# Optimization experiments

Measured on AMD Instinct MI355X. Metric: run time of the kernel, lower is better.

The kernel has to match this reference:

```python
import jax, jax.numpy as jnp
import numpy as np

B, DZ, DS, DH = 8192, 1024, 64, 4096

def setup_inputs() -> dict:
    key = jax.random.key(0)
    ks = jax.random.split(key, 8)
    r1 = 1.0 / np.sqrt(DZ)   # W1 init range (last dim dz)
    r2 = 1.0 / np.sqrt(DH)   # W2 init range (last dim dim_hidden)
    rc = 1.0 / np.sqrt(DS)   # C init range
    return {
        "z": jax.random.normal(ks[0], (B, DZ), jnp.float32),
        "s": jax.random.normal(ks[1], (B, DS), jnp.float32),
        "A": jnp.full((DZ,), 0.95, jnp.float32),
        "W1": jax.random.uniform(ks[2], (DH, DZ), jnp.float32, -r1, r1),
        "W2": jax.random.uniform(ks[3], (DZ, DH), jnp.float32, -r2, r2),
        "h1": jax.random.normal(ks[4], (DH,), jnp.float32),
        "h2": jax.random.normal(ks[5], (DZ,), jnp.float32),
        "C": jax.random.uniform(ks[6], (DZ, DS), jnp.float32, -rc, rc),
    }

def reference(z, s, A, W1, W2, h1, h2, C):
    # PLRNN step, W_trial=False, mean_center=False, noise=0:
    # z' = A*z + relu(z @ W1.T + h1) @ W2.T + h2 + s @ C.T
    z_activated = jax.nn.relu(z @ W1.T + h1)          # [B, DH]
    return A * z + z_activated @ W2.T + h2 + s @ C.T  # [B, DZ]
```

## Files before the change

### kernel.cpp

```cpp
#include <hip/hip_runtime.h>

#define BB 8192
#define DZ 1024
#define DS 64
#define DH 4096
#define KEXT (DH + DS)

typedef float floatx4 __attribute__((ext_vector_type(4)));
typedef __bf16 bf16x8 __attribute__((ext_vector_type(8)));
typedef __attribute__((address_space(1))) void* as1_void_ptr;
typedef __attribute__((address_space(3))) void* as3_void_ptr;

__device__ __forceinline__ void async_copy16(const void* g, void* l) {
    __builtin_amdgcn_global_load_lds((as1_void_ptr)g, (as3_void_ptr)l, 16, 0, 0);
}

__global__ void prep_all(const float* __restrict__ z, const float* __restrict__ W1,
                         const float* __restrict__ W2, const float* __restrict__ C,
                         const float* __restrict__ s,
                         __bf16* __restrict__ zb, __bf16* __restrict__ W1b,
                         __bf16* __restrict__ B2b, __bf16* __restrict__ Hb) {
    const int b = blockIdx.x, t = threadIdx.x;
    if (b < 8192) {
        int i = b * 256 + t;
        float4 v = ((const float4*)z)[i];
        __bf16* o = zb + (size_t)i * 4;
        o[0] = (__bf16)v.x; o[1] = (__bf16)v.y; o[2] = (__bf16)v.z; o[3] = (__bf16)v.w;
    } else if (b < 12288) {
        int i = (b - 8192) * 256 + t;
        float4 v = ((const float4*)W1)[i];
        __bf16* o = W1b + (size_t)i * 4;
        o[0] = (__bf16)v.x; o[1] = (__bf16)v.y; o[2] = (__bf16)v.z; o[3] = (__bf16)v.w;
    } else if (b < 13312) {
        int j = b - 12288;
        for (int h = t; h < KEXT; h += 256) {
            float v = (h < DH) ? W2[(size_t)j * DH + h] : C[(size_t)j * DS + (h - DH)];
            B2b[(size_t)j * KEXT + h] = (__bf16)v;
        }
    } else {
        int i = (b - 13312) * 256 + t;
        int r = i >> 6, k = i & 63;
        Hb[(size_t)r * KEXT + DH + k] = (__bf16)s[i];
    }
}


__global__ __launch_bounds__(256) void gemm1_relu(
    const __bf16* __restrict__ Ag, const __bf16* __restrict__ Bg,
    const float* __restrict__ h1, __bf16* __restrict__ Hb)
{
    constexpr int ldA = DZ, ldB = DZ, KITER = DZ / 64;
    __shared__ __align__(16) __bf16 As[2 * 128 * 32];
    __shared__ __align__(16) __bf16 Bs[2 * 128 * 32];

    const int tid = threadIdx.x;
    const int wave = tid >> 6, lane = tid & 63;
    const int wm = wave >> 1, wn = wave & 1;
    const int row0 = blockIdx.x * 128;
    const int col0 = blockIdx.y * 128;

    const __bf16* pA = Ag + (size_t)(row0 + (tid >> 2)) * ldA + (tid & 3) * 8;
    const __bf16* pB = Bg + (size_t)(col0 + (tid >> 2)) * ldB + (tid & 3) * 8;
    __bf16* dA0 = As + wave * 16 * 32;
    __bf16* dB0 = Bs + wave * 16 * 32;

    const __bf16* Afrag = As + (wm * 64 + (lane & 15)) * 32 + (lane >> 4) * 8;
    const __bf16* Bfrag = Bs + (wn * 64 + (lane & 15)) * 32 + (lane >> 4) * 8;

    floatx4 acc[4][4];
#pragma unroll
    for (int i = 0; i < 4; ++i)
#pragma unroll
        for (int j = 0; j < 4; ++j) acc[i][j] = (floatx4)0.0f;

    for (int kt = 0; kt < KITER; ++kt) {
        const __bf16* ak = pA + kt * 64;
        const __bf16* bk = pB + kt * 64;
        async_copy16(ak,                         dA0);
        async_copy16(ak + (size_t)64 * ldA,      dA0 + 64 * 32);
        async_copy16(ak + 32,                    dA0 + 128 * 32);
        async_copy16(ak + (size_t)64 * ldA + 32, dA0 + 128 * 32 + 64 * 32);
        async_copy16(bk,                         dB0);
        async_copy16(bk + (size_t)64 * ldB,      dB0 + 64 * 32);
        async_copy16(bk + 32,                    dB0 + 128 * 32);
        async_copy16(bk + (size_t)64 * ldB + 32, dB0 + 128 * 32 + 64 * 32);
        __builtin_amdgcn_s_waitcnt(0);
        __syncthreads();

#pragma unroll
        for (int ks = 0; ks < 2; ++ks) {
            bf16x8 af[4], bfr[4];
#pragma unroll
            for (int i = 0; i < 4; ++i) af[i] = *(const bf16x8*)(Afrag + ks * 4096 + i * 16 * 32);
#pragma unroll
            for (int j = 0; j < 4; ++j) bfr[j] = *(const bf16x8*)(Bfrag + ks * 4096 + j * 16 * 32);
#pragma unroll
            for (int i = 0; i < 4; ++i)
#pragma unroll
                for (int j = 0; j < 4; ++j)
                    acc[i][j] = __builtin_amdgcn_mfma_f32_16x16x32_bf16(af[i], bfr[j], acc[i][j], 0, 0, 0);
        }
        __syncthreads();
    }

    const int r0 = row0 + wm * 64 + (lane >> 4) * 4;
    const int c0 = col0 + wn * 64 + (lane & 15);
#pragma unroll
    for (int i = 0; i < 4; ++i) {
#pragma unroll
        for (int j = 0; j < 4; ++j) {
            int c = c0 + j * 16;
            float bias = h1[c];
#pragma unroll
            for (int rg = 0; rg < 4; ++rg) {
                int r = r0 + i * 16 + rg;
                float v = acc[i][j][rg] + bias;
                v = v > 0.0f ? v : 0.0f;
                Hb[(size_t)r * KEXT + c] = (__bf16)v;
            }
        }
    }
}

__global__ __launch_bounds__(256) void gemm2_out(
    const __bf16* __restrict__ Ag, const __bf16* __restrict__ Bg,
    const float* __restrict__ Adiag, const float* __restrict__ h2,
    const __bf16* __restrict__ zb, float* __restrict__ out)
{
    constexpr int ldA = KEXT, ldB = KEXT, KITER = KEXT / 64;
    __shared__ __align__(16) __bf16 As[2 * 128 * 32];
    __shared__ __align__(16) __bf16 Bs[2 * 128 * 32];

    const int tid = threadIdx.x;
    const int wave = tid >> 6, lane = tid & 63;
    const int wm = wave >> 1, wn = wave & 1;
    const int row0 = blockIdx.x * 128;
    const int col0 = blockIdx.y * 128;

    const __bf16* pA = Ag + (size_t)(row0 + (tid >> 2)) * ldA + (tid & 3) * 8;
    const __bf16* pB = Bg + (size_t)(col0 + (tid >> 2)) * ldB + (tid & 3) * 8;
    __bf16* dA0 = As + wave * 16 * 32;
    __bf16* dB0 = Bs + wave * 16 * 32;

    const __bf16* Afrag = As + (wm * 64 + (lane & 15)) * 32 + (lane >> 4) * 8;
    const __bf16* Bfrag = Bs + (wn * 64 + (lane & 15)) * 32 + (lane >> 4) * 8;

    floatx4 acc[4][4];
#pragma unroll
    for (int i = 0; i < 4; ++i)
#pragma unroll
        for (int j = 0; j < 4; ++j) acc[i][j] = (floatx4)0.0f;

    for (int kt = 0; kt < KITER; ++kt) {
        const __bf16* ak = pA + kt * 64;
        const __bf16* bk = pB + kt * 64;
        async_copy16(ak,                         dA0);
        async_copy16(ak + (size_t)64 * ldA,      dA0 + 64 * 32);
        async_copy16(ak + 32,                    dA0 + 128 * 32);
        async_copy16(ak + (size_t)64 * ldA + 32, dA0 + 128 * 32 + 64 * 32);
        async_copy16(bk,                         dB0);
        async_copy16(bk + (size_t)64 * ldB,      dB0 + 64 * 32);
        async_copy16(bk + 32,                    dB0 + 128 * 32);
        async_copy16(bk + (size_t)64 * ldB + 32, dB0 + 128 * 32 + 64 * 32);
        __builtin_amdgcn_s_waitcnt(0);
        __syncthreads();

#pragma unroll
        for (int ks = 0; ks < 2; ++ks) {
            bf16x8 af[4], bfr[4];
#pragma unroll
            for (int i = 0; i < 4; ++i) af[i] = *(const bf16x8*)(Afrag + ks * 4096 + i * 16 * 32);
#pragma unroll
            for (int j = 0; j < 4; ++j) bfr[j] = *(const bf16x8*)(Bfrag + ks * 4096 + j * 16 * 32);
#pragma unroll
            for (int i = 0; i < 4; ++i)
#pragma unroll
                for (int j = 0; j < 4; ++j)
                    acc[i][j] = __builtin_amdgcn_mfma_f32_16x16x32_bf16(af[i], bfr[j], acc[i][j], 0, 0, 0);
        }
        __syncthreads();
    }

    const int r0 = row0 + wm * 64 + (lane >> 4) * 4;
    const int c0 = col0 + wn * 64 + (lane & 15);
#pragma unroll
    for (int i = 0; i < 4; ++i) {
#pragma unroll
        for (int j = 0; j < 4; ++j) {
            const int c = c0 + j * 16;
            const float aj = Adiag[c];
            const float hj = h2[c];
#pragma unroll
            for (int rg = 0; rg < 4; ++rg) {
                const int r = r0 + i * 16 + rg;
                out[(size_t)r * DZ + c] =
                    acc[i][j][rg] + aj * (float)zb[(size_t)r * DZ + c] + hj;
            }
        }
    }
}


extern "C" void kernel_launch(void* const* d_in, const int* in_sizes, int n_in,
                              void* d_out, int out_size, void* d_ws, size_t ws_size,
                              hipStream_t stream) {
    const float* z  = (const float*)d_in[0];
    const float* s  = (const float*)d_in[1];
    const float* A  = (const float*)d_in[2];
    const float* W1 = (const float*)d_in[3];
    const float* W2 = (const float*)d_in[4];
    const float* h1 = (const float*)d_in[5];
    const float* h2 = (const float*)d_in[6];
    const float* C  = (const float*)d_in[7];
    float* out = (float*)d_out;

    char* ws = (char*)d_ws;
    size_t offHb  = 0;
    size_t offZb  = offHb  + (size_t)BB * KEXT * 2;
    size_t offW1b = offZb  + (size_t)BB * DZ * 2;
    size_t offB2b = offW1b + (size_t)DH * DZ * 2;
    __bf16* Hb  = (__bf16*)(ws + offHb);
    __bf16* zb  = (__bf16*)(ws + offZb);
    __bf16* W1b = (__bf16*)(ws + offW1b);
    __bf16* B2b = (__bf16*)(ws + offB2b);

    prep_all<<<15360, 256, 0, stream>>>(z, W1, W2, C, s, zb, W1b, B2b, Hb);
    gemm1_relu<<<dim3(BB / 128, DH / 128), 256, 0, stream>>>(zb, W1b, h1, Hb);
    gemm2_out<<<dim3(BB / 128, DZ / 128), 256, 0, stream>>>(Hb, B2b, A, h2, zb, out);
}
```

Baseline: 282.2 us.

## Double-buffer GEMM K-loop with swizzled LDS and 32x32 MFMA tiles

Both GEMM kernels now share a pipelined mainloop that prefetches the next 32-wide K slice into an alternate LDS buffer while computing on the current one, waiting on a partial vmcnt instead of draining all loads. The LDS layout uses an XOR chunk swizzle to reduce bank conflicts on fragment reads, and the MFMA switches from 16x16x32 to 32x32x16 with a 2x2 accumulator grid per wave. The epilogues are remapped to the 32x32 output layout. The goal is to hide global-load latency and cut LDS traffic per MFMA, at the cost of halving K per iteration (more barriers) and relying on hand-encoded waitcnt constants.

```diff
diff --git a/kernel.cpp b/kernel.cpp
--- a/kernel.cpp
+++ b/kernel.cpp
@@ -6,10 +6,14 @@
 #define DH 4096
 #define KEXT (DH + DS)
 
-typedef float floatx4 __attribute__((ext_vector_type(4)));
+typedef float floatx16 __attribute__((ext_vector_type(16)));
 typedef __bf16 bf16x8 __attribute__((ext_vector_type(8)));
 typedef __attribute__((address_space(1))) void* as1_void_ptr;
 typedef __attribute__((address_space(3))) void* as3_void_ptr;
+
+#define WAIT_VM4   3956
+#define WAIT_VM0   3952
+#define WAIT_LGKM0 49279
 
 __device__ __forceinline__ void async_copy16(const void* g, void* l) {
     __builtin_amdgcn_global_load_lds((as1_void_ptr)g, (as3_void_ptr)l, 16, 0, 0);
@@ -45,78 +49,94 @@
 }
 
 
+
+#define GEMM_PIPELINE_BODY(KITER_, ldA_, ldB_)                                          \
+    const int tid = threadIdx.x;                                                        \
+    const int wave = tid >> 6, lane = tid & 63;                                         \
+    const int wm = wave >> 1, wn = wave & 1;                                            \
+    const int row0 = blockIdx.x * 128;                                                  \
+    const int col0 = blockIdx.y * 128;                                                  \
+    const int srow = tid >> 2;                                   \
+    const int schk = (tid & 3) ^ (srow & 3);                 \
+    const __bf16* pA = Ag + (size_t)(row0 + srow) * ldA_ + schk * 8;                    \
+    const __bf16* pB = Bg + (size_t)(col0 + srow) * ldB_ + schk * 8;                    \
+    const int mA = lane & 31, hA = lane >> 5;                                           \
+    floatx16 acc[2][2];                                                                 \
+    acc[0][0] = (floatx16)0.0f; acc[0][1] = (floatx16)0.0f;                             \
+    acc[1][0] = (floatx16)0.0f; acc[1][1] = (floatx16)0.0f;                             \
+    {                                         \
+        __bf16* lA = As + wave * 512;                                                   \
+        __bf16* lB = Bs + wave * 512;                                                   \
+        async_copy16(pA,                    lA);                                        \
+        async_copy16(pA + (size_t)64*ldA_,  lA + 2048);                                 \
+        async_copy16(pB,                    lB);                                        \
+        async_copy16(pB + (size_t)64*ldB_,  lB + 2048);                                 \
+    }                                                                                   \
+    for (int kt = 0; kt < KITER_; ++kt) {                                               \
+        const int p = kt & 1;                                                           \
+        if (kt + 1 < KITER_) {                                                          \
+            const __bf16* ak = pA + (kt + 1) * 32;                                      \
+            const __bf16* bk = pB + (kt + 1) * 32;                                      \
+            __bf16* lA = As + (p ^ 1) * 4096 + wave * 512;                              \
+            __bf16* lB = Bs + (p ^ 1) * 4096 + wave * 512;                              \
+            async_copy16(ak,                    lA);                                    \
+            async_copy16(ak + (size_t)64*ldA_,  lA + 2048);                             \
+            async_copy16(bk,                    lB);                                    \
+            async_copy16(bk + (size_t)64*ldB_,  lB + 2048);                             \
+            __builtin_amdgcn_s_waitcnt(WAIT_VM4);                                       \
+        } else {                                                                        \
+            __builtin_amdgcn_s_waitcnt(WAIT_VM0);                                       \
+        }                                                                               \
+        __builtin_amdgcn_s_barrier();                                                   \
+        const __bf16* Ab = As + p * 4096;                                               \
+        const __bf16* Bb = Bs + p * 4096;                                               \
+        _Pragma("unroll")                                                               \
+        for (int ks = 0; ks < 2; ++ks) {                                                \
+            bf16x8 af[2], bf[2];                                                        \
+            _Pragma("unroll")                                                           \
+            for (int i = 0; i < 2; ++i) {                                               \
+                int r = wm * 64 + i * 32 + mA;                                          \
+                int chunk = (ks * 2 + hA) ^ (mA & 3);                                   \
+                af[i] = *(const bf16x8*)(Ab + r * 32 + chunk * 8);                      \
+            }                                                                           \
+            _Pragma("unroll")                                                           \
+            for (int j = 0; j < 2; ++j) {                                               \
+                int r = wn * 64 + j * 32 + mA;                                          \
+                int chunk = (ks * 2 + hA) ^ (mA & 3);                                   \
+                bf[j] = *(const bf16x8*)(Bb + r * 32 + chunk * 8);                      \
+            }                                                                           \
+            _Pragma("unroll")                                                           \
+            for (int i = 0; i < 2; ++i)                                                 \
+                _Pragma("unroll")                                                       \
+                for (int j = 0; j < 2; ++j)                                             \
+                    acc[i][j] = __builtin_amdgcn_mfma_f32_32x32x16_bf16(                \
+                        af[i], bf[j], acc[i][j], 0, 0, 0);                              \
+        }                                                                               \
+        __builtin_amdgcn_s_waitcnt(WAIT_LGKM0);                                         \
+        __builtin_amdgcn_s_barrier();                                                   \
+    }
+
 __global__ __launch_bounds__(256) void gemm1_relu(
     const __bf16* __restrict__ Ag, const __bf16* __restrict__ Bg,
     const float* __restrict__ h1, __bf16* __restrict__ Hb)
 {
-    constexpr int ldA = DZ, ldB = DZ, KITER = DZ / 64;
     __shared__ __align__(16) __bf16 As[2 * 128 * 32];
     __shared__ __align__(16) __bf16 Bs[2 * 128 * 32];
 
-    const int tid = threadIdx.x;
-    const int wave = tid >> 6, lane = tid & 63;
-    const int wm = wave >> 1, wn = wave & 1;
-    const int row0 = blockIdx.x * 128;
-    const int col0 = blockIdx.y * 128;
-
-    const __bf16* pA = Ag + (size_t)(row0 + (tid >> 2)) * ldA + (tid & 3) * 8;
-    const __bf16* pB = Bg + (size_t)(col0 + (tid >> 2)) * ldB + (tid & 3) * 8;
-    __bf16* dA0 = As + wave * 16 * 32;
-    __bf16* dB0 = Bs + wave * 16 * 32;
-
-    const __bf16* Afrag = As + (wm * 64 + (lane & 15)) * 32 + (lane >> 4) * 8;
-    const __bf16* Bfrag = Bs + (wn * 64 + (lane & 15)) * 32 + (lane >> 4) * 8;
-
-    floatx4 acc[4][4];
-#pragma unroll
-    for (int i = 0; i < 4; ++i)
-#pragma unroll
-        for (int j = 0; j < 4; ++j) acc[i][j] = (floatx4)0.0f;
-
-    for (int kt = 0; kt < KITER; ++kt) {
-        const __bf16* ak = pA + kt * 64;
-        const __bf16* bk = pB + kt * 64;
-        async_copy16(ak,                         dA0);
-        async_copy16(ak + (size_t)64 * ldA,      dA0 + 64 * 32);
-        async_copy16(ak + 32,                    dA0 + 128 * 32);
-        async_copy16(ak + (size_t)64 * ldA + 32, dA0 + 128 * 32 + 64 * 32);
-        async_copy16(bk,                         dB0);
-        async_copy16(bk + (size_t)64 * ldB,      dB0 + 64 * 32);
-        async_copy16(bk + 32,                    dB0 + 128 * 32);
-        async_copy16(bk + (size_t)64 * ldB + 32, dB0 + 128 * 32 + 64 * 32);
-        __builtin_amdgcn_s_waitcnt(0);
-        __syncthreads();
+    GEMM_PIPELINE_BODY(32, DZ, DZ)
 
 #pragma unroll
-        for (int ks = 0; ks < 2; ++ks) {
-            bf16x8 af[4], bfr[4];
+    for (int i = 0; i < 2; ++i) {
 #pragma unroll
-            for (int i = 0; i < 4; ++i) af[i] = *(const bf16x8*)(Afrag + ks * 4096 + i * 16 * 32);
+        for (int j = 0; j < 2; ++j) {
+            const int cbase = col0 + wn * 64 + j * 32 + mA;
+            const float bias = h1[cbase];
 #pragma unroll
-            for (int j = 0; j < 4; ++j) bfr[j] = *(const bf16x8*)(Bfrag + ks * 4096 + j * 16 * 32);
-#pragma unroll
-            for (int i = 0; i < 4; ++i)
-#pragma unroll
-                for (int j = 0; j < 4; ++j)
-                    acc[i][j] = __builtin_amdgcn_mfma_f32_16x16x32_bf16(af[i], bfr[j], acc[i][j], 0, 0, 0);
-        }
-        __syncthreads();
-    }
-
-    const int r0 = row0 + wm * 64 + (lane >> 4) * 4;
-    const int c0 = col0 + wn * 64 + (lane & 15);
-#pragma unroll
-    for (int i = 0; i < 4; ++i) {
-#pragma unroll
-        for (int j = 0; j < 4; ++j) {
-            int c = c0 + j * 16;
-            float bias = h1[c];
-#pragma unroll
-            for (int rg = 0; rg < 4; ++rg) {
-                int r = r0 + i * 16 + rg;
+            for (int rg = 0; rg < 16; ++rg) {
+                const int r = row0 + wm * 64 + i * 32 + (rg & 3) + 8 * (rg >> 2) + 4 * hA;
                 float v = acc[i][j][rg] + bias;
                 v = v > 0.0f ? v : 0.0f;
-                Hb[(size_t)r * KEXT + c] = (__bf16)v;
+                Hb[(size_t)r * KEXT + cbase] = (__bf16)v;
             }
         }
     }
@@ -127,72 +147,21 @@
     const float* __restrict__ Adiag, const float* __restrict__ h2,
     const __bf16* __restrict__ zb, float* __restrict__ out)
 {
-    constexpr int ldA = KEXT, ldB = KEXT, KITER = KEXT / 64;
     __shared__ __align__(16) __bf16 As[2 * 128 * 32];
     __shared__ __align__(16) __bf16 Bs[2 * 128 * 32];
 
-    const int tid = threadIdx.x;
-    const int wave = tid >> 6, lane = tid & 63;
-    const int wm = wave >> 1, wn = wave & 1;
-    const int row0 = blockIdx.x * 128;
-    const int col0 = blockIdx.y * 128;
-
-    const __bf16* pA = Ag + (size_t)(row0 + (tid >> 2)) * ldA + (tid & 3) * 8;
-    const __bf16* pB = Bg + (size_t)(col0 + (tid >> 2)) * ldB + (tid & 3) * 8;
-    __bf16* dA0 = As + wave * 16 * 32;
-    __bf16* dB0 = Bs + wave * 16 * 32;
-
-    const __bf16* Afrag = As + (wm * 64 + (lane & 15)) * 32 + (lane >> 4) * 8;
-    const __bf16* Bfrag = Bs + (wn * 64 + (lane & 15)) * 32 + (lane >> 4) * 8;
-
-    floatx4 acc[4][4];
-#pragma unroll
-    for (int i = 0; i < 4; ++i)
-#pragma unroll
-        for (int j = 0; j < 4; ++j) acc[i][j] = (floatx4)0.0f;
-
-    for (int kt = 0; kt < KITER; ++kt) {
-        const __bf16* ak = pA + kt * 64;
-        const __bf16* bk = pB + kt * 64;
-        async_copy16(ak,                         dA0);
-        async_copy16(ak + (size_t)64 * ldA,      dA0 + 64 * 32);
-        async_copy16(ak + 32,                    dA0 + 128 * 32);
-        async_copy16(ak + (size_t)64 * ldA + 32, dA0 + 128 * 32 + 64 * 32);
-        async_copy16(bk,                         dB0);
-        async_copy16(bk + (size_t)64 * ldB,      dB0 + 64 * 32);
-        async_copy16(bk + 32,                    dB0 + 128 * 32);
-        async_copy16(bk + (size_t)64 * ldB + 32, dB0 + 128 * 32 + 64 * 32);
-        __builtin_amdgcn_s_waitcnt(0);
-        __syncthreads();
+    GEMM_PIPELINE_BODY(130, KEXT, KEXT)
 
 #pragma unroll
-        for (int ks = 0; ks < 2; ++ks) {
-            bf16x8 af[4], bfr[4];
+    for (int i = 0; i < 2; ++i) {
 #pragma unroll
-            for (int i = 0; i < 4; ++i) af[i] = *(const bf16x8*)(Afrag + ks * 4096 + i * 16 * 32);
-#pragma unroll
-            for (int j = 0; j < 4; ++j) bfr[j] = *(const bf16x8*)(Bfrag + ks * 4096 + j * 16 * 32);
-#pragma unroll
-            for (int i = 0; i < 4; ++i)
-#pragma unroll
-                for (int j = 0; j < 4; ++j)
-                    acc[i][j] = __builtin_amdgcn_mfma_f32_16x16x32_bf16(af[i], bfr[j], acc[i][j], 0, 0, 0);
-        }
-        __syncthreads();
-    }
-
-    const int r0 = row0 + wm * 64 + (lane >> 4) * 4;
-    const int c0 = col0 + wn * 64 + (lane & 15);
-#pragma unroll
-    for (int i = 0; i < 4; ++i) {
-#pragma unroll
-        for (int j = 0; j < 4; ++j) {
-            const int c = c0 + j * 16;
+        for (int j = 0; j < 2; ++j) {
+            const int c = col0 + wn * 64 + j * 32 + mA;
             const float aj = Adiag[c];
             const float hj = h2[c];
 #pragma unroll
-            for (int rg = 0; rg < 4; ++rg) {
-                const int r = r0 + i * 16 + rg;
+            for (int rg = 0; rg < 16; ++rg) {
+                const int r = row0 + wm * 64 + i * 32 + (rg & 3) + 8 * (rg >> 2) + 4 * hA;
                 out[(size_t)r * DZ + c] =
                     acc[i][j][rg] + aj * (float)zb[(size_t)r * DZ + c] + hj;
             }
```

Result: slower. 304.7 us (+8.0%).

## Double-buffer LDS tiles with async prefetch in both GEMM kernels

Applied to the files above, without the earlier changes.

Both GEMM main loops now prefetch the next K-tile into a second LDS buffer with global_load_lds, then wait only on older vmem loads via partial vmcnt waits before a raw barrier. gemm1 switches to 32-wide K steps so its double-buffered tile fits the existing LDS allocation, while gemm2 doubles its LDS to hold two 64-wide K-tiles. The aim is to overlap global-to-LDS copies with MFMA work instead of fully draining memory every iteration. The risks are fragile hand-encoded waitcnt constants, more barriers per K in gemm1, and higher LDS use in gemm2 that may reduce occupancy.

```diff
diff --git a/kernel.cpp b/kernel.cpp
--- a/kernel.cpp
+++ b/kernel.cpp
@@ -10,6 +10,11 @@
 typedef __bf16 bf16x8 __attribute__((ext_vector_type(8)));
 typedef __attribute__((address_space(1))) void* as1_void_ptr;
 typedef __attribute__((address_space(3))) void* as3_void_ptr;
+
+#define WAIT_VM0   3952
+#define WAIT_VM4   3956
+#define WAIT_VM8   3960
+#define WAIT_LGKM0 49279
 
 __device__ __forceinline__ void async_copy16(const void* g, void* l) {
     __builtin_amdgcn_global_load_lds((as1_void_ptr)g, (as3_void_ptr)l, 16, 0, 0);
@@ -49,7 +54,7 @@
     const __bf16* __restrict__ Ag, const __bf16* __restrict__ Bg,
     const float* __restrict__ h1, __bf16* __restrict__ Hb)
 {
-    constexpr int ldA = DZ, ldB = DZ, KITER = DZ / 64;
+    constexpr int ldA = DZ, ldB = DZ, KITER = DZ / 32;
     __shared__ __align__(16) __bf16 As[2 * 128 * 32];
     __shared__ __align__(16) __bf16 Bs[2 * 128 * 32];
 
@@ -61,8 +66,6 @@
 
     const __bf16* pA = Ag + (size_t)(row0 + (tid >> 2)) * ldA + (tid & 3) * 8;
     const __bf16* pB = Bg + (size_t)(col0 + (tid >> 2)) * ldB + (tid & 3) * 8;
-    __bf16* dA0 = As + wave * 16 * 32;
-    __bf16* dB0 = Bs + wave * 16 * 32;
 
     const __bf16* Afrag = As + (wm * 64 + (lane & 15)) * 32 + (lane >> 4) * 8;
     const __bf16* Bfrag = Bs + (wn * 64 + (lane & 15)) * 32 + (lane >> 4) * 8;
@@ -73,34 +76,47 @@
 #pragma unroll
         for (int j = 0; j < 4; ++j) acc[i][j] = (floatx4)0.0f;
 
+    {
+        __bf16* lA = As + wave * 512;
+        __bf16* lB = Bs + wave * 512;
+        async_copy16(pA,                        lA);
+        async_copy16(pA + (size_t)64 * ldA,     lA + 2048);
+        async_copy16(pB,                        lB);
+        async_copy16(pB + (size_t)64 * ldB,     lB + 2048);
+    }
+
     for (int kt = 0; kt < KITER; ++kt) {
-        const __bf16* ak = pA + kt * 64;
-        const __bf16* bk = pB + kt * 64;
-        async_copy16(ak,                         dA0);
-        async_copy16(ak + (size_t)64 * ldA,      dA0 + 64 * 32);
-        async_copy16(ak + 32,                    dA0 + 128 * 32);
-        async_copy16(ak + (size_t)64 * ldA + 32, dA0 + 128 * 32 + 64 * 32);
-        async_copy16(bk,                         dB0);
-        async_copy16(bk + (size_t)64 * ldB,      dB0 + 64 * 32);
-        async_copy16(bk + 32,                    dB0 + 128 * 32);
-        async_copy16(bk + (size_t)64 * ldB + 32, dB0 + 128 * 32 + 64 * 32);
-        __builtin_amdgcn_s_waitcnt(0);
-        __syncthreads();
-
-#pragma unroll
-        for (int ks = 0; ks < 2; ++ks) {
-            bf16x8 af[4], bfr[4];
-#pragma unroll
-            for (int i = 0; i < 4; ++i) af[i] = *(const bf16x8*)(Afrag + ks * 4096 + i * 16 * 32);
-#pragma unroll
-            for (int j = 0; j < 4; ++j) bfr[j] = *(const bf16x8*)(Bfrag + ks * 4096 + j * 16 * 32);
-#pragma unroll
-            for (int i = 0; i < 4; ++i)
-#pragma unroll
-                for (int j = 0; j < 4; ++j)
-                    acc[i][j] = __builtin_amdgcn_mfma_f32_16x16x32_bf16(af[i], bfr[j], acc[i][j], 0, 0, 0);
-        }
-        __syncthreads();
+        const int p = kt & 1;
+        if (kt + 1 < KITER) {
+            const __bf16* ak = pA + (kt + 1) * 32;
+            const __bf16* bk = pB + (kt + 1) * 32;
+            __bf16* lA = As + (p ^ 1) * 4096 + wave * 512;
+            __bf16* lB = Bs + (p ^ 1) * 4096 + wave * 512;
+            async_copy16(ak,                    lA);
+            async_copy16(ak + (size_t)64 * ldA, lA + 2048);
+            async_copy16(bk,                    lB);
+            async_copy16(bk + (size_t)64 * ldB, lB + 2048);
+            __builtin_amdgcn_s_waitcnt(WAIT_VM4);
+        } else {
+            __builtin_amdgcn_s_waitcnt(WAIT_VM0);
+        }
+        __builtin_amdgcn_s_barrier();
+
+        const __bf16* Ab = Afrag + p * 4096;
+        const __bf16* Bb = Bfrag + p * 4096;
+        bf16x8 af[4], bfr[4];
+#pragma unroll
+        for (int i = 0; i < 4; ++i) af[i] = *(const bf16x8*)(Ab + i * 16 * 32);
+#pragma unroll
+        for (int j = 0; j < 4; ++j) bfr[j] = *(const bf16x8*)(Bb + j * 16 * 32);
+#pragma unroll
+        for (int i = 0; i < 4; ++i)
+#pragma unroll
+            for (int j = 0; j < 4; ++j)
+                acc[i][j] = __builtin_amdgcn_mfma_f32_16x16x32_bf16(af[i], bfr[j], acc[i][j], 0, 0, 0);
+
+        __builtin_amdgcn_s_waitcnt(WAIT_LGKM0);
+        __builtin_amdgcn_s_barrier();
     }
 
     const int r0 = row0 + wm * 64 + (lane >> 4) * 4;
@@ -128,8 +144,8 @@
     const __bf16* __restrict__ zb, float* __restrict__ out)
 {
     constexpr int ldA = KEXT, ldB = KEXT, KITER = KEXT / 64;
-    __shared__ __align__(16) __bf16 As[2 * 128 * 32];
-    __shared__ __align__(16) __bf16 Bs[2 * 128 * 32];
+    __shared__ __align__(16) __bf16 As[2 * 2 * 128 * 32];
+    __shared__ __align__(16) __bf16 Bs[2 * 2 * 128 * 32];
 
     const int tid = threadIdx.x;
     const int wave = tid >> 6, lane = tid & 63;
@@ -139,8 +155,6 @@
 
     const __bf16* pA = Ag + (size_t)(row0 + (tid >> 2)) * ldA + (tid & 3) * 8;
     const __bf16* pB = Bg + (size_t)(col0 + (tid >> 2)) * ldB + (tid & 3) * 8;
-    __bf16* dA0 = As + wave * 16 * 32;
-    __bf16* dB0 = Bs + wave * 16 * 32;
 
     const __bf16* Afrag = As + (wm * 64 + (lane & 15)) * 32 + (lane >> 4) * 8;
     const __bf16* Bfrag = Bs + (wn * 64 + (lane & 15)) * 32 + (lane >> 4) * 8;
@@ -151,34 +165,58 @@
 #pragma unroll
         for (int j = 0; j < 4; ++j) acc[i][j] = (floatx4)0.0f;
 
+    {
+        __bf16* lA = As + wave * 512;
+        __bf16* lB = Bs + wave * 512;
+        async_copy16(pA,                             lA);
+        async_copy16(pA + (size_t)64 * ldA,          lA + 2048);
+        async_copy16(pA + 32,                        lA + 4096);
+        async_copy16(pA + (size_t)64 * ldA + 32,     lA + 4096 + 2048);
+        async_copy16(pB,                             lB);
+        async_copy16(pB + (size_t)64 * ldB,          lB + 2048);
+        async_copy16(pB + 32,                        lB + 4096);
+        async_copy16(pB + (size_t)64 * ldB + 32,     lB + 4096 + 2048);
+    }
+
     for (int kt = 0; kt < KITER; ++kt) {
-        const __bf16* ak = pA + kt * 64;
-        const __bf16* bk = pB + kt * 64;
-        async_copy16(ak,                         dA0);
-        async_copy16(ak + (size_t)64 * ldA,      dA0 + 64 * 32);
-        async_copy16(ak + 32,                    dA0 + 128 * 32);
-        async_copy16(ak + (size_t)64 * ldA + 32, dA0 + 128 * 32 + 64 * 32);
-        async_copy16(bk,                         dB0);
-        async_copy16(bk + (size_t)64 * ldB,      dB0 + 64 * 32);
-        async_copy16(bk + 32,                    dB0 + 128 * 32);
-        async_copy16(bk + (size_t)64 * ldB + 32, dB0 + 128 * 32 + 64 * 32);
-        __builtin_amdgcn_s_waitcnt(0);
-        __syncthreads();
+        const int p = kt & 1;
+        if (kt + 1 < KITER) {
+            const __bf16* ak = pA + (kt + 1) * 64;
+            const __bf16* bk = pB + (kt + 1) * 64;
+            __bf16* lA = As + (p ^ 1) * 8192 + wave * 512;
+            __bf16* lB = Bs + (p ^ 1) * 8192 + wave * 512;
+            async_copy16(ak,                         lA);
+            async_copy16(ak + (size_t)64 * ldA,      lA + 2048);
+            async_copy16(ak + 32,                    lA + 4096);
+            async_copy16(ak + (size_t)64 * ldA + 32, lA + 4096 + 2048);
+            async_copy16(bk,                         lB);
+            async_copy16(bk + (size_t)64 * ldB,      lB + 2048);
+            async_copy16(bk + 32,                    lB + 4096);
+            async_copy16(bk + (size_t)64 * ldB + 32, lB + 4096 + 2048);
+            __builtin_amdgcn_s_waitcnt(WAIT_VM8);
+        } else {
+            __builtin_amdgcn_s_waitcnt(WAIT_VM0);
+        }
+        __builtin_amdgcn_s_barrier();
 
 #pragma unroll
         for (int ks = 0; ks < 2; ++ks) {
+            const __bf16* Ab = Afrag + p * 8192 + ks * 4096;
+            const __bf16* Bb = Bfrag + p * 8192 + ks * 4096;
             bf16x8 af[4], bfr[4];
 #pragma unroll
-            for (int i = 0; i < 4; ++i) af[i] = *(const bf16x8*)(Afrag + ks * 4096 + i * 16 * 32);
-#pragma unroll
-            for (int j = 0; j < 4; ++j) bfr[j] = *(const bf16x8*)(Bfrag + ks * 4096 + j * 16 * 32);
+            for (int i = 0; i < 4; ++i) af[i] = *(const bf16x8*)(Ab + i * 16 * 32);
+#pragma unroll
+            for (int j = 0; j < 4; ++j) bfr[j] = *(const bf16x8*)(Bb + j * 16 * 32);
 #pragma unroll
             for (int i = 0; i < 4; ++i)
 #pragma unroll
                 for (int j = 0; j < 4; ++j)
                     acc[i][j] = __builtin_amdgcn_mfma_f32_16x16x32_bf16(af[i], bfr[j], acc[i][j], 0, 0, 0);
         }
-        __syncthreads();
+
+        __builtin_amdgcn_s_waitcnt(WAIT_LGKM0);
+        __builtin_amdgcn_s_barrier();
     }
 
     const int r0 = row0 + wm * 64 + (lane >> 4) * 4;
```

Result: slower. 294.1 us (+4.2%).
